# Kernel optimization log

Hardware: AMD Instinct MI355X
Metric: run time of the kernel (lower is better)

## Reference

```python
import jax, jax.numpy as jnp
import numpy as np

B, N, C = 8, 4096, 512
H, DK, DV = 8, 64, 64


def _xnorm(x, gamma):
    # L2 norm over last dim, keepdim; scale by per-head gamma
    nrm = jnp.sqrt(jnp.sum(x * x, axis=-1, keepdims=True))
    return x * gamma / nrm


def setup_inputs() -> dict:
    key = jax.random.key(0)
    ks = jax.random.split(key, 9)
    inp = {
        "queries": jax.random.normal(ks[0], (B, N, C), dtype=jnp.float32),
        "keys": jax.random.normal(ks[1], (B, N, C), dtype=jnp.float32),
        "values": jax.random.normal(ks[2], (B, N, C), dtype=jnp.float32),
        # Linear weights stored torch-style [out, in]; init.normal_(std=0.001), bias=0
        "Wq": jax.random.normal(ks[3], (H * DK, C), dtype=jnp.float32) * 0.001,
        "bq": jnp.zeros((H * DK,), dtype=jnp.float32),
        "Wk": jax.random.normal(ks[4], (H * DK, C), dtype=jnp.float32) * 0.001,
        "bk": jnp.zeros((H * DK,), dtype=jnp.float32),
        "Wv": jax.random.normal(ks[5], (H * DV, C), dtype=jnp.float32) * 0.001,
        "bv": jnp.zeros((H * DV,), dtype=jnp.float32),
        "Wo": jax.random.normal(ks[6], (C, H * DV), dtype=jnp.float32) * 0.001,
        "bo": jnp.zeros((C,), dtype=jnp.float32),
        "gamma": jax.random.normal(ks[7], (1, H, 1, 1), dtype=jnp.float32),
    }
    return inp


def reference(queries, keys, values, Wq, bq, Wk, bk, Wv, bv, Wo, bo, gamma):
    bs, nq, _ = queries.shape
    nk = keys.shape[1]
    # projections -> [b, h, n, d]
    q = (queries @ Wq.T + bq).reshape(bs, nq, H, DK).transpose(0, 2, 1, 3)
    k = (keys @ Wk.T + bk).reshape(bs, nk, H, DK).transpose(0, 2, 1, 3)
    v = (values @ Wv.T + bv).reshape(bs, nk, H, DV).transpose(0, 2, 1, 3)
    # kv: [b, h, dk, dv]  (small intermediate)
    kv = jnp.einsum('bhnk,bhnv->bhkv', k, v)
    kv_n = _xnorm(kv, gamma)     # norm over dv
    q_n = _xnorm(q, gamma)       # norm over dk
    out = jnp.einsum('bhnk,bhkv->bhnv', q_n, kv_n)  # [b,h,nq,dv]
    out = out.transpose(0, 2, 1, 3).reshape(bs, nq, H * DV)
    return out @ Wo.T + bo
```

## Files before the change

kernel.cpp:

```cpp
#include <hip/hip_runtime.h>


typedef __attribute__((ext_vector_type(4))) float f32x4;
typedef __attribute__((ext_vector_type(8))) short s16x8;
typedef __attribute__((ext_vector_type(4))) unsigned short u16x4;
typedef __attribute__((ext_vector_type(8))) unsigned short u16x8;

#define DEVFN __device__ __forceinline__

DEVFN unsigned short f2b(float f) {
  union { float f; unsigned u; } un; un.f = f;
  unsigned r = un.u + 0x7fffu + ((un.u >> 16) & 1u);
  return (unsigned short)(r >> 16);
}
DEVFN float b2f(unsigned short us) {
  union { unsigned u; float f; } un; un.u = ((unsigned)us) << 16;
  return un.f;
}

template <bool AF32, typename CT>
DEVFN void gemm_core(const void* Ain, const unsigned short* Bt,
                     const float* bias, CT* C, bool qnorm, const float* gamma,
                     int bx, int by) {
  constexpr int KK = 512, NN = 512;
  __shared__ unsigned short As[2][128 * 64];
  __shared__ unsigned short Bs[2][128 * 64];
  const int tid = threadIdx.x, lane = tid & 63, wid = tid >> 6;
  const int wm = (wid >> 1) * 64, wn = (wid & 1) * 64;
  const int r = lane & 15, g = lane >> 4;

  const float* Af = nullptr;
  const unsigned short* Ab = nullptr;
  if constexpr (AF32)
    Af = (const float*)Ain + (long)(bx * 128 + (tid >> 4)) * KK + (tid & 15) * 4;
  else
    Ab = (const unsigned short*)Ain + (long)(bx * 128 + (tid >> 3)) * KK + (tid & 7) * 8;
  const unsigned short* Bp = Bt + (long)(by * 128 + (tid >> 3)) * KK + (tid & 7) * 8;

  f32x4 PAf0[8], PAf1[8];
  u16x8 PAb0[4], PAb1[4];
  u16x8 PB0[4], PB1[4];
  f32x4 acc[4][4] = {};

#define ISSUE(SET, KT)                                                         \
  {                                                                            \
    if constexpr (AF32) {                                                      \
      _Pragma("unroll") for (int i = 0; i < 8; ++i)                            \
          PAf##SET[i] = *reinterpret_cast<const f32x4*>(                       \
              Af + (long)i * 16 * KK + (KT)*64);                               \
    } else {                                                                   \
      _Pragma("unroll") for (int i = 0; i < 4; ++i)                            \
          PAb##SET[i] = *reinterpret_cast<const u16x8*>(                       \
              Ab + (long)i * 32 * KK + (KT)*64);                               \
    }                                                                          \
    _Pragma("unroll") for (int i = 0; i < 4; ++i)                              \
        PB##SET[i] = *reinterpret_cast<const u16x8*>(                          \
            Bp + (long)i * 32 * KK + (KT)*64);                                 \
  }

#define WRITE(SET, BUF)                                                        \
  {                                                                            \
    if constexpr (AF32) {                                                      \
      const int rr = tid >> 4, cb = (tid & 15) * 8;                            \
      _Pragma("unroll") for (int i = 0; i < 8; ++i) {                          \
        int row = i * 16 + rr;                                                 \
        int off = row * 128 + (cb ^ ((row & 7) << 4));                         \
        u16x4 o = {f2b(PAf##SET[i][0]), f2b(PAf##SET[i][1]),                   \
                   f2b(PAf##SET[i][2]), f2b(PAf##SET[i][3])};                  \
        *reinterpret_cast<u16x4*>(reinterpret_cast<char*>(As[BUF]) + off) = o; \
      }                                                                        \
    } else {                                                                   \
      const int rr = tid >> 3, cb = (tid & 7) * 16;                            \
      _Pragma("unroll") for (int i = 0; i < 4; ++i) {                          \
        int row = i * 32 + rr;                                                 \
        int off = row * 128 + (cb ^ ((row & 7) << 4));                         \
        *reinterpret_cast<u16x8*>(reinterpret_cast<char*>(As[BUF]) + off) =    \
            PAb##SET[i];                                                       \
      }                                                                        \
    }                                                                          \
    {                                                                          \
      const int rr = tid >> 3, cb = (tid & 7) * 16;                            \
      _Pragma("unroll") for (int i = 0; i < 4; ++i) {                          \
        int row = i * 32 + rr;                                                 \
        int off = row * 128 + (cb ^ ((row & 7) << 4));                         \
        *reinterpret_cast<u16x8*>(reinterpret_cast<char*>(Bs[BUF]) + off) =    \
            PB##SET[i];                                                        \
      }                                                                        \
    }                                                                          \
  }

#define COMPUTE(BUF)                                                           \
  {                                                                            \
    _Pragma("unroll") for (int ks = 0; ks < 2; ++ks) {                         \
      s16x8 a[4], b[4];                                                        \
      const int kb = ks * 64 + g * 16;                                         \
      _Pragma("unroll") for (int i = 0; i < 4; ++i) {                          \
        int ar = wm + i * 16 + r;                                              \
        a[i] = *reinterpret_cast<const s16x8*>(                                \
            reinterpret_cast<char*>(As[BUF]) + ar * 128 +                      \
            (kb ^ ((ar & 7) << 4)));                                           \
        int br = wn + i * 16 + r;                                              \
        b[i] = *reinterpret_cast<const s16x8*>(                                \
            reinterpret_cast<char*>(Bs[BUF]) + br * 128 +                      \
            (kb ^ ((br & 7) << 4)));                                           \
      }                                                                        \
      _Pragma("unroll") for (int i = 0; i < 4; ++i)                            \
          _Pragma("unroll") for (int j = 0; j < 4; ++j) acc[i][j] =            \
          __builtin_amdgcn_mfma_f32_16x16x32_bf16(a[i], b[j], acc[i][j], 0,    \
                                                  0, 0);                       \
    }                                                                          \
  }

#define WAITBAR                                                                \
  asm volatile("s_waitcnt lgkmcnt(0)" ::: "memory");                           \
  __builtin_amdgcn_sched_barrier(0);                                           \
  __builtin_amdgcn_s_barrier();                                                \
  __builtin_amdgcn_sched_barrier(0);

#define SB0 __builtin_amdgcn_sched_barrier(0);

  ISSUE(0, 0)
  ISSUE(1, 1)
  WRITE(0, 0)
  WAITBAR
  ISSUE(0, 2) SB0 COMPUTE(0) WRITE(1, 1) WAITBAR
  ISSUE(1, 3) SB0 COMPUTE(1) WRITE(0, 0) WAITBAR
  ISSUE(0, 4) SB0 COMPUTE(0) WRITE(1, 1) WAITBAR
  ISSUE(1, 5) SB0 COMPUTE(1) WRITE(0, 0) WAITBAR
  ISSUE(0, 6) SB0 COMPUTE(0) WRITE(1, 1) WAITBAR
  ISSUE(1, 7) SB0 COMPUTE(1) WRITE(0, 0) WAITBAR
  COMPUTE(0) WRITE(1, 1) WAITBAR
  COMPUTE(1)

#undef ISSUE
#undef WRITE
#undef COMPUTE
#undef WAITBAR
#undef SB0

  const int crow0 = bx * 128 + wm + g * 4;
  const int ccol0 = by * 128 + wn + r;
#pragma unroll
  for (int j = 0; j < 4; ++j) {
    float bv = bias[ccol0 + j * 16];
#pragma unroll
    for (int i = 0; i < 4; ++i)
#pragma unroll
      for (int ii = 0; ii < 4; ++ii) acc[i][j][ii] += bv;
  }
  if (qnorm) {
    const int h = (by * 128 + wn) >> 6;
    const float gam = gamma[h];
#pragma unroll
    for (int i = 0; i < 4; ++i)
#pragma unroll
      for (int ii = 0; ii < 4; ++ii) {
        float s = 0.f;
#pragma unroll
        for (int j = 0; j < 4; ++j) s += acc[i][j][ii] * acc[i][j][ii];
        s += __shfl_xor(s, 1);
        s += __shfl_xor(s, 2);
        s += __shfl_xor(s, 4);
        s += __shfl_xor(s, 8);
        float sc = gam / sqrtf(s);
#pragma unroll
        for (int j = 0; j < 4; ++j) acc[i][j][ii] *= sc;
      }
  }
#pragma unroll
  for (int i = 0; i < 4; ++i)
#pragma unroll
    for (int j = 0; j < 4; ++j)
#pragma unroll
      for (int ii = 0; ii < 4; ++ii) {
        long row = crow0 + i * 16 + ii;
        int col = ccol0 + j * 16;
        if constexpr (sizeof(CT) == 2)
          C[row * NN + col] = f2b(acc[i][j][ii]);
        else
          C[row * NN + col] = acc[i][j][ii];
      }
}

DEVFN void swz_xy(int bid, int nwg, int& bx, int& by) {
  int s = (bid & 7) * (nwg >> 3) + (bid >> 3);
  bx = s >> 2;
  by = s & 3;
}

__global__ __launch_bounds__(256, 2)
void proj_qkv(const float* __restrict__ Aq, const float* __restrict__ Ak,
              const float* __restrict__ Av, const unsigned short* __restrict__ Bq,
              const unsigned short* __restrict__ Bk, const unsigned short* __restrict__ Bv,
              const float* __restrict__ bq, const float* __restrict__ bk,
              const float* __restrict__ bv, unsigned short* __restrict__ Cq,
              unsigned short* __restrict__ Ck, unsigned short* __restrict__ Cv,
              const float* __restrict__ gamma) {
  const int z = blockIdx.z;
  const float* A = z == 0 ? Aq : (z == 1 ? Ak : Av);
  const unsigned short* B = z == 0 ? Bq : (z == 1 ? Bk : Bv);
  const float* bias = z == 0 ? bq : (z == 1 ? bk : bv);
  unsigned short* C = z == 0 ? Cq : (z == 1 ? Ck : Cv);
  int bx, by;
  swz_xy(blockIdx.x, 1024, bx, by);
  gemm_core<true, unsigned short>(A, B, bias, C, z == 0, gamma, bx, by);
}

__global__ __launch_bounds__(256, 2)
void gemm_final(const unsigned short* __restrict__ q, const unsigned short* __restrict__ Mt,
                const float* __restrict__ bo, float* __restrict__ out) {
  const int zb = blockIdx.z;
  int bx, by;
  swz_xy(blockIdx.x, 128, bx, by);
  gemm_core<false, float>(q + (long)zb * 2097152, Mt + (long)zb * 262144, bo,
                          out + (long)zb * 2097152, false, nullptr, bx, by);
}

#define NCHUNK 16
__global__ __launch_bounds__(256, 2)
void kv_partial(const unsigned short* __restrict__ kq,
                const unsigned short* __restrict__ vq,
                float* __restrict__ part) {
  const int tid = threadIdx.x;
  const int chunk = blockIdx.x;
  const int bh = blockIdx.y;
  const int b = bh >> 3, h = bh & 7;
  __shared__ float ks[32][64];
  __shared__ float vs[32][64];
  const int dk0 = (tid & 15) * 4;
  const int dv0 = (tid >> 4) * 4;
  float acc[4][4] = {};
  const long nbase = (long)b * 4096 + chunk * 256;

  for (int sub = 0; sub < 8; ++sub) {
    long n0 = nbase + sub * 32;
#pragma unroll
    for (int i = 0; i < 2; ++i) {
      int e = i * 256 + tid;
      int row = e >> 4, c4 = e & 15;
      long gofs = (n0 + row) * 512 + h * 64 + c4 * 4;
      u16x4 kk = *reinterpret_cast<const u16x4*>(kq + gofs);
      u16x4 vv = *reinterpret_cast<const u16x4*>(vq + gofs);
      f32x4 kf = {b2f(kk[0]), b2f(kk[1]), b2f(kk[2]), b2f(kk[3])};
      f32x4 vf = {b2f(vv[0]), b2f(vv[1]), b2f(vv[2]), b2f(vv[3])};
      *reinterpret_cast<f32x4*>(&ks[row][c4 * 4]) = kf;
      *reinterpret_cast<f32x4*>(&vs[row][c4 * 4]) = vf;
    }
    __syncthreads();
#pragma unroll 4
    for (int n = 0; n < 32; ++n) {
      f32x4 kk = *reinterpret_cast<const f32x4*>(&ks[n][dk0]);
      f32x4 vv = *reinterpret_cast<const f32x4*>(&vs[n][dv0]);
#pragma unroll
      for (int a = 0; a < 4; ++a)
#pragma unroll
        for (int c = 0; c < 4; ++c)
          acc[a][c] += kk[a] * vv[c];
    }
    __syncthreads();
  }
  float* pg = part + ((long)chunk * 64 + bh) * 4096;
#pragma unroll
  for (int a = 0; a < 4; ++a) {
    f32x4 o = {acc[a][0], acc[a][1], acc[a][2], acc[a][3]};
    *reinterpret_cast<f32x4*>(pg + (dk0 + a) * 64 + dv0) = o;
  }
}

__global__ __launch_bounds__(256)
void kv_normN(const float* __restrict__ part, const float* __restrict__ gamma,
              unsigned short* __restrict__ kvn) {
  const int bh = blockIdx.x, h = bh & 7;
  const int tid = threadIdx.x;
  __shared__ float kvs[4096];
  __shared__ float scale[64];
#pragma unroll
  for (int i = 0; i < 4; ++i) {
    int e4 = i * 256 + tid;
    const float* p = part + (long)bh * 4096 + e4 * 4;
    f32x4 s = {0.f, 0.f, 0.f, 0.f};
#pragma unroll
    for (int c = 0; c < NCHUNK; ++c) {
      f32x4 v = *reinterpret_cast<const f32x4*>(p + (long)c * 64 * 4096);
      s += v;
    }
    *reinterpret_cast<f32x4*>(kvs + e4 * 4) = s;
  }
  __syncthreads();
  if (tid < 64) {
    float s = 0.f;
    for (int dv = 0; dv < 64; ++dv) { float x = kvs[tid * 64 + dv]; s += x * x; }
    scale[tid] = gamma[h] / sqrtf(s);
  }
  __syncthreads();
#pragma unroll
  for (int i = 0; i < 4; ++i) {
    int e4 = i * 256 + tid;
    float sc = scale[e4 >> 4];
    f32x4 v = *reinterpret_cast<const f32x4*>(kvs + e4 * 4);
    u16x4 o = {f2b(v[0] * sc), f2b(v[1] * sc), f2b(v[2] * sc), f2b(v[3] * sc)};
    *reinterpret_cast<u16x4*>(kvn + (long)bh * 4096 + e4 * 4) = o;
  }
}

__global__ __launch_bounds__(64)
void mt_kernel(const unsigned short* __restrict__ Wo_b,
               const unsigned short* __restrict__ kvn,
               unsigned short* __restrict__ Mt) {
  const int bid = blockIdx.x;
  const int bh = bid >> 2, seg = bid & 3;
  const int b = bh >> 3, h = bh & 7;
  const int lane = threadIdx.x;
  const int r = lane & 15, g = lane >> 4;
  f32x4 acc[8][4] = {};
  s16x8 bf[2][4];
#pragma unroll
  for (int ks = 0; ks < 2; ++ks)
#pragma unroll
    for (int j = 0; j < 4; ++j)
      bf[ks][j] = *reinterpret_cast<const s16x8*>(
          kvn + (long)bh * 4096 + (j * 16 + r) * 64 + ks * 32 + g * 8);
#pragma unroll
  for (int ks = 0; ks < 2; ++ks)
#pragma unroll
    for (int i = 0; i < 8; ++i) {
      s16x8 af = *reinterpret_cast<const s16x8*>(
          Wo_b + (long)(seg * 128 + i * 16 + r) * 512 + h * 64 + ks * 32 + g * 8);
#pragma unroll
      for (int j = 0; j < 4; ++j)
        acc[i][j] = __builtin_amdgcn_mfma_f32_16x16x32_bf16(af, bf[ks][j], acc[i][j], 0, 0, 0);
    }
#pragma unroll
  for (int i = 0; i < 8; ++i)
#pragma unroll
    for (int j = 0; j < 4; ++j)
#pragma unroll
      for (int ii = 0; ii < 4; ++ii) {
        int c = seg * 128 + i * 16 + g * 4 + ii;
        int dk = j * 16 + r;
        Mt[(long)b * 262144 + (long)c * 512 + h * 64 + dk] = f2b(acc[i][j][ii]);
      }
}

__global__ void cast4(const float* __restrict__ a0, const float* __restrict__ a1,
                      const float* __restrict__ a2, const float* __restrict__ a3,
                      unsigned short* __restrict__ o0, unsigned short* __restrict__ o1,
                      unsigned short* __restrict__ o2, unsigned short* __restrict__ o3) {
  const int y = blockIdx.y;
  const float* in = y == 0 ? a0 : (y == 1 ? a1 : (y == 2 ? a2 : a3));
  unsigned short* out = y == 0 ? o0 : (y == 1 ? o1 : (y == 2 ? o2 : o3));
  int i = blockIdx.x * 256 + threadIdx.x;
  f32x4 v = reinterpret_cast<const f32x4*>(in)[i];
  reinterpret_cast<u16x4*>(out)[i] = u16x4{f2b(v[0]), f2b(v[1]), f2b(v[2]), f2b(v[3])};
}

extern "C" void kernel_launch(void* const* d_in, const int* in_sizes, int n_in,
                              void* d_out, int out_size, void* d_ws, size_t ws_size,
                              hipStream_t stream) {
  const float* queries = (const float*)d_in[0];
  const float* keys    = (const float*)d_in[1];
  const float* values  = (const float*)d_in[2];
  const float* Wq = (const float*)d_in[3];
  const float* bq = (const float*)d_in[4];
  const float* Wk = (const float*)d_in[5];
  const float* bk = (const float*)d_in[6];
  const float* Wv = (const float*)d_in[7];
  const float* bv = (const float*)d_in[8];
  const float* Wo = (const float*)d_in[9];
  const float* bo = (const float*)d_in[10];
  const float* gamma = (const float*)d_in[11];

  unsigned short* Wq_b = (unsigned short*)d_ws;
  unsigned short* Wk_b = Wq_b + 262144;
  unsigned short* Wv_b = Wk_b + 262144;
  unsigned short* Wo_b = Wv_b + 262144;
  unsigned short* q_b  = Wo_b + 262144;
  unsigned short* kvn  = q_b + 16777216;
  float* part = (float*)(kvn + 262144);
  unsigned short* Mt = (unsigned short*)part;
  unsigned short* k_b = (unsigned short*)d_out;
  unsigned short* v_b = k_b + 16777216;
  float* out = (float*)d_out;

  cast4<<<dim3(256, 4), 256, 0, stream>>>(Wq, Wk, Wv, Wo, Wq_b, Wk_b, Wv_b, Wo_b);

  proj_qkv<<<dim3(1024, 1, 3), 256, 0, stream>>>(
      queries, keys, values, Wq_b, Wk_b, Wv_b, bq, bk, bv, q_b, k_b, v_b, gamma);

  kv_partial<<<dim3(NCHUNK, 64), 256, 0, stream>>>(k_b, v_b, part);
  kv_normN<<<64, 256, 0, stream>>>(part, gamma, kvn);
  mt_kernel<<<256, 64, 0, stream>>>(Wo_b, kvn, Mt);

  gemm_final<<<dim3(128, 1, 8), 256, 0, stream>>>(q_b, Mt, bo, out);
}
```

Before: 186.2 us.

## Single-buffer A tile and single prefetch register set to raise GEMM occupancy

The shared GEMM core now keeps only one LDS buffer for the A tile while B stays double-buffered, and holds a single set of prefetch registers instead of two. The pipeline is reordered to compute, write B into the alternate buffer, barrier, then overwrite A, and launch bounds rise from 2 to 3 blocks per CU. The aim is lower LDS and register use so more waves stay resident to hide memory latency. In exchange, each k-step gets an extra barrier, prefetch depth drops from two tiles to one, and a tighter register budget could cause spills.

```diff
diff --git a/kernel.cpp b/kernel.cpp
--- a/kernel.cpp
+++ b/kernel.cpp
@@ -23,7 +23,7 @@
                      const float* bias, CT* C, bool qnorm, const float* gamma,
                      int bx, int by) {
   constexpr int KK = 512, NN = 512;
-  __shared__ unsigned short As[2][128 * 64];
+  __shared__ unsigned short As[128 * 64];
   __shared__ unsigned short Bs[2][128 * 64];
   const int tid = threadIdx.x, lane = tid & 63, wid = tid >> 6;
   const int wm = (wid >> 1) * 64, wn = (wid & 1) * 64;
@@ -37,59 +37,60 @@
     Ab = (const unsigned short*)Ain + (long)(bx * 128 + (tid >> 3)) * KK + (tid & 7) * 8;
   const unsigned short* Bp = Bt + (long)(by * 128 + (tid >> 3)) * KK + (tid & 7) * 8;
 
-  f32x4 PAf0[8], PAf1[8];
-  u16x8 PAb0[4], PAb1[4];
-  u16x8 PB0[4], PB1[4];
+  f32x4 PAf[8];
+  u16x8 PAb[4];
+  u16x8 PB[4];
   f32x4 acc[4][4] = {};
 
-#define ISSUE(SET, KT)                                                         \
+#define ISSUE(KT)                                                              \
   {                                                                            \
+    _Pragma("unroll") for (int i = 0; i < 4; ++i)                              \
+        PB[i] = *reinterpret_cast<const u16x8*>(                               \
+            Bp + (long)i * 32 * KK + (KT)*64);                                 \
     if constexpr (AF32) {                                                      \
       _Pragma("unroll") for (int i = 0; i < 8; ++i)                            \
-          PAf##SET[i] = *reinterpret_cast<const f32x4*>(                       \
+          PAf[i] = *reinterpret_cast<const f32x4*>(                            \
               Af + (long)i * 16 * KK + (KT)*64);                               \
     } else {                                                                   \
       _Pragma("unroll") for (int i = 0; i < 4; ++i)                            \
-          PAb##SET[i] = *reinterpret_cast<const u16x8*>(                       \
+          PAb[i] = *reinterpret_cast<const u16x8*>(                            \
               Ab + (long)i * 32 * KK + (KT)*64);                               \
     }                                                                          \
-    _Pragma("unroll") for (int i = 0; i < 4; ++i)                              \
-        PB##SET[i] = *reinterpret_cast<const u16x8*>(                          \
-            Bp + (long)i * 32 * KK + (KT)*64);                                 \
-  }
-
-#define WRITE(SET, BUF)                                                        \
+  }
+
+#define WRITE_A                                                                \
   {                                                                            \
     if constexpr (AF32) {                                                      \
       const int rr = tid >> 4, cb = (tid & 15) * 8;                            \
       _Pragma("unroll") for (int i = 0; i < 8; ++i) {                          \
         int row = i * 16 + rr;                                                 \
         int off = row * 128 + (cb ^ ((row & 7) << 4));                         \
-        u16x4 o = {f2b(PAf##SET[i][0]), f2b(PAf##SET[i][1]),                   \
-                   f2b(PAf##SET[i][2]), f2b(PAf##SET[i][3])};                  \
-        *reinterpret_cast<u16x4*>(reinterpret_cast<char*>(As[BUF]) + off) = o; \
+        u16x4 o = {f2b(PAf[i][0]), f2b(PAf[i][1]),                             \
+                   f2b(PAf[i][2]), f2b(PAf[i][3])};                            \
+        *reinterpret_cast<u16x4*>(reinterpret_cast<char*>(As) + off) = o;      \
       }                                                                        \
     } else {                                                                   \
       const int rr = tid >> 3, cb = (tid & 7) * 16;                            \
       _Pragma("unroll") for (int i = 0; i < 4; ++i) {                          \
         int row = i * 32 + rr;                                                 \
         int off = row * 128 + (cb ^ ((row & 7) << 4));                         \
-        *reinterpret_cast<u16x8*>(reinterpret_cast<char*>(As[BUF]) + off) =    \
-            PAb##SET[i];                                                       \
+        *reinterpret_cast<u16x8*>(reinterpret_cast<char*>(As) + off) = PAb[i]; \
       }                                                                        \
     }                                                                          \
-    {                                                                          \
-      const int rr = tid >> 3, cb = (tid & 7) * 16;                            \
-      _Pragma("unroll") for (int i = 0; i < 4; ++i) {                          \
-        int row = i * 32 + rr;                                                 \
-        int off = row * 128 + (cb ^ ((row & 7) << 4));                         \
-        *reinterpret_cast<u16x8*>(reinterpret_cast<char*>(Bs[BUF]) + off) =    \
-            PB##SET[i];                                                        \
-      }                                                                        \
+  }
+
+#define WRITE_B(BUF)                                                           \
+  {                                                                            \
+    const int rr = tid >> 3, cb = (tid & 7) * 16;                              \
+    _Pragma("unroll") for (int i = 0; i < 4; ++i) {                            \
+      int row = i * 32 + rr;                                                   \
+      int off = row * 128 + (cb ^ ((row & 7) << 4));                           \
+      *reinterpret_cast<u16x8*>(reinterpret_cast<char*>(Bs[BUF]) + off) =      \
+          PB[i];                                                               \
     }                                                                          \
   }
 
-#define COMPUTE(BUF)                                                           \
+#define COMPUTE(BBUF)                                                          \
   {                                                                            \
     _Pragma("unroll") for (int ks = 0; ks < 2; ++ks) {                         \
       s16x8 a[4], b[4];                                                        \
@@ -97,11 +98,11 @@
       _Pragma("unroll") for (int i = 0; i < 4; ++i) {                          \
         int ar = wm + i * 16 + r;                                              \
         a[i] = *reinterpret_cast<const s16x8*>(                                \
-            reinterpret_cast<char*>(As[BUF]) + ar * 128 +                      \
+            reinterpret_cast<const char*>(As) + ar * 128 +                     \
             (kb ^ ((ar & 7) << 4)));                                           \
         int br = wn + i * 16 + r;                                              \
         b[i] = *reinterpret_cast<const s16x8*>(                                \
-            reinterpret_cast<char*>(Bs[BUF]) + br * 128 +                      \
+            reinterpret_cast<const char*>(Bs[BBUF]) + br * 128 +               \
             (kb ^ ((br & 7) << 4)));                                           \
       }                                                                        \
       _Pragma("unroll") for (int i = 0; i < 4; ++i)                            \
@@ -111,31 +112,32 @@
     }                                                                          \
   }
 
-#define WAITBAR                                                                \
+#define SB0 __builtin_amdgcn_sched_barrier(0);
+#define BAR_RAW                                                                \
+  SB0 __builtin_amdgcn_s_barrier(); SB0
+#define LGKM_BAR                                                               \
   asm volatile("s_waitcnt lgkmcnt(0)" ::: "memory");                           \
-  __builtin_amdgcn_sched_barrier(0);                                           \
-  __builtin_amdgcn_s_barrier();                                                \
-  __builtin_amdgcn_sched_barrier(0);
-
-#define SB0 __builtin_amdgcn_sched_barrier(0);
-
-  ISSUE(0, 0)
-  ISSUE(1, 1)
-  WRITE(0, 0)
-  WAITBAR
-  ISSUE(0, 2) SB0 COMPUTE(0) WRITE(1, 1) WAITBAR
-  ISSUE(1, 3) SB0 COMPUTE(1) WRITE(0, 0) WAITBAR
-  ISSUE(0, 4) SB0 COMPUTE(0) WRITE(1, 1) WAITBAR
-  ISSUE(1, 5) SB0 COMPUTE(1) WRITE(0, 0) WAITBAR
-  ISSUE(0, 6) SB0 COMPUTE(0) WRITE(1, 1) WAITBAR
-  ISSUE(1, 7) SB0 COMPUTE(1) WRITE(0, 0) WAITBAR
-  COMPUTE(0) WRITE(1, 1) WAITBAR
+  SB0 __builtin_amdgcn_s_barrier(); SB0
+
+  ISSUE(0)
+  WRITE_B(0)
+  WRITE_A
+  LGKM_BAR
+  ISSUE(1) SB0 COMPUTE(0) WRITE_B(1) BAR_RAW WRITE_A LGKM_BAR
+  ISSUE(2) SB0 COMPUTE(1) WRITE_B(0) BAR_RAW WRITE_A LGKM_BAR
+  ISSUE(3) SB0 COMPUTE(0) WRITE_B(1) BAR_RAW WRITE_A LGKM_BAR
+  ISSUE(4) SB0 COMPUTE(1) WRITE_B(0) BAR_RAW WRITE_A LGKM_BAR
+  ISSUE(5) SB0 COMPUTE(0) WRITE_B(1) BAR_RAW WRITE_A LGKM_BAR
+  ISSUE(6) SB0 COMPUTE(1) WRITE_B(0) BAR_RAW WRITE_A LGKM_BAR
+  ISSUE(7) SB0 COMPUTE(0) WRITE_B(1) BAR_RAW WRITE_A LGKM_BAR
   COMPUTE(1)
 
 #undef ISSUE
-#undef WRITE
+#undef WRITE_A
+#undef WRITE_B
 #undef COMPUTE
-#undef WAITBAR
+#undef BAR_RAW
+#undef LGKM_BAR
 #undef SB0
 
   const int crow0 = bx * 128 + wm + g * 4;
@@ -188,7 +190,7 @@
   by = s & 3;
 }
 
-__global__ __launch_bounds__(256, 2)
+__global__ __launch_bounds__(256, 3)
 void proj_qkv(const float* __restrict__ Aq, const float* __restrict__ Ak,
               const float* __restrict__ Av, const unsigned short* __restrict__ Bq,
               const unsigned short* __restrict__ Bk, const unsigned short* __restrict__ Bv,
@@ -206,7 +208,7 @@
   gemm_core<true, unsigned short>(A, B, bias, C, z == 0, gamma, bx, by);
 }
 
-__global__ __launch_bounds__(256, 2)
+__global__ __launch_bounds__(256, 3)
 void gemm_final(const unsigned short* __restrict__ q, const unsigned short* __restrict__ Mt,
                 const float* __restrict__ bo, float* __restrict__ out) {
   const int zb = blockIdx.z;
```

Result: slower. 240.1 us (+28.9%).
